# Kernel optimization log

Hardware: AMD Instinct MI355X
Metric: run time of the kernel (lower is better)

Reference implementation:

```python
import jax, jax.numpy as jnp
import numpy as np

B, S, D, H = 4, 1024, 1024, 16
DK = D // H


def _rel_shift(x):
    # Transformer-XL relative shift: x is (b, h, t1, t2) with t1 == t2
    b, h, t1, t2 = x.shape
    x = jnp.pad(x, ((0, 0), (0, 0), (0, 0), (1, 0)))  # pad left of last dim
    x = x.reshape(b, h, t2 + 1, t1)
    return x[:, :, 1:, :].reshape(b, h, t1, t2)


def setup_inputs() -> dict:
    rng = jax.random.key(0)
    ks = jax.random.split(rng, 10)
    w = 0.02
    return {
        "query": jax.random.normal(ks[0], (B, S, D), jnp.float32),
        "key": jax.random.normal(ks[1], (B, S, D), jnp.float32),
        "value": jax.random.normal(ks[2], (B, S, D), jnp.float32),
        "mask": jnp.ones((B, S), dtype=bool),
        "Wq": jax.random.normal(ks[3], (D, D), jnp.float32) * w,
        "Wk": jax.random.normal(ks[4], (D, D), jnp.float32) * w,
        "Wv": jax.random.normal(ks[5], (D, D), jnp.float32) * w,
        "Wp": jax.random.normal(ks[6], (D, D), jnp.float32) * w,
        "Wo": jax.random.normal(ks[7], (D, D), jnp.float32) * w,
        "pos_bias_u": jax.random.normal(ks[8], (H, DK), jnp.float32) * w,
        "pos_bias_v": jax.random.normal(ks[9], (H, DK), jnp.float32) * w,
    }


def reference(query, key, value, mask, Wq, Wk, Wv, Wp, Wo, pos_bias_u, pos_bias_v):
    b, s, dm = query.shape
    h, dk = pos_bias_u.shape

    # sinusoidal relative position embeddings (positions s-1 ... 0)
    inv_freq = 1.0 / (10000.0 ** (jnp.arange(0, dm, 2, dtype=jnp.float32) / dm))
    pos_seq = jnp.arange(s - 1, -1, -1, dtype=jnp.float32)
    sin_inp = pos_seq[:, None] * inv_freq[None, :]              # (s, dm/2)
    pos_emb = jnp.concatenate([jnp.sin(sin_inp), jnp.cos(sin_inp)], -1)  # (s, dm)

    # projections (torch Linear: y = x @ W.T)
    q = (query @ Wq.T).reshape(b, s, h, dk).transpose(0, 2, 1, 3)  # (b,h,s,dk)
    k = (key @ Wk.T).reshape(b, s, h, dk).transpose(0, 2, 1, 3)
    v = (value @ Wv.T).reshape(b, s, h, dk).transpose(0, 2, 1, 3)
    p = (pos_emb @ Wp.T).reshape(s, h, dk).transpose(1, 0, 2)       # (h,s,dk), same for all batches

    content_score = jnp.einsum('bhqd,bhkd->bhqk', q + pos_bias_u[None, :, None, :], k)
    pos_score = jnp.einsum('bhqd,hkd->bhqk', q + pos_bias_v[None, :, None, :], p)
    pos_score = _rel_shift(pos_score)

    scores = (content_score + pos_score) / jnp.sqrt(jnp.float32(dk))
    attn_mask = mask[:, None, :, None] & mask[:, None, None, :]    # (b,1,q,k)
    scores = jnp.where(attn_mask, scores, jnp.float32(-1e9))

    attn = jax.nn.softmax(scores, axis=-1)  # dropout is identity at eval
    context = jnp.einsum('bhqk,bhkd->bqhd', attn, v).reshape(b, s, dm)
    return context @ Wo.T
```

## Files before the change

kernel.cpp:

```cpp
#include <hip/hip_runtime.h>
#include <math.h>

#define BATCH 4
#define SEQ   1024
#define DM    1024
#define NH    16
#define DK    64

typedef __attribute__((ext_vector_type(8))) short short8;
typedef __attribute__((ext_vector_type(4))) float f32x4;

__device__ inline unsigned short f2bf(float f) {
    unsigned u = __float_as_uint(f);
    unsigned r = (u + 0x7fffu + ((u >> 16) & 1u)) >> 16;
    return (unsigned short)r;
}
__device__ inline float bf2f(unsigned short s) {
    return __uint_as_float(((unsigned)s) << 16);
}
__device__ inline void split1(float x, unsigned short& h, unsigned short& l) {
    h = f2bf(x);
    l = f2bf(x - bf2f(h));
}

__global__ __launch_bounds__(256) void cvt_split(const float4* __restrict__ x,
                                                 ushort4* __restrict__ h,
                                                 ushort4* __restrict__ l, int n4) {
    int i = blockIdx.x * blockDim.x + threadIdx.x;
    if (i >= n4) return;
    float4 v = x[i];
    ushort4 hv, lv;
    split1(v.x, hv.x, lv.x);
    split1(v.y, hv.y, lv.y);
    split1(v.z, hv.z, lv.z);
    split1(v.w, hv.w, lv.w);
    h[i] = hv;
    l[i] = lv;
}

__global__ void posemb_kernel(unsigned short* __restrict__ peh,
                              unsigned short* __restrict__ pel) {
    int idx = blockIdx.x * blockDim.x + threadIdx.x;
    if (idx >= SEQ * DM) return;
    int j = idx / DM, d = idx % DM;
    double pos = (double)(SEQ - 1 - j);
    int i = (d < DM / 2) ? d : d - DM / 2;
    double inv_freq = exp(-((2.0 * (double)i) / (double)DM) * log(10000.0));
    double a = pos * inv_freq;
    float v = (d < DM / 2) ? (float)sin(a) : (float)cos(a);
    unsigned short hh, ll;
    split1(v, hh, ll);
    peh[idx] = hh;
    pel[idx] = ll;
}

__global__ __launch_bounds__(256) void prep_q(const float4* __restrict__ qp4,
                                              const float4* __restrict__ ub4,
                                              const float4* __restrict__ vb4,
                                              ushort4* __restrict__ quh,
                                              ushort4* __restrict__ qul,
                                              ushort4* __restrict__ qvh,
                                              ushort4* __restrict__ qvl) {
    int i = blockIdx.x * 256 + threadIdx.x;
    float4 q = qp4[i];
    int dm4 = i & (DM / 4 - 1);
    float4 u = ub4[dm4], v = vb4[dm4];
    ushort4 h, l;
    split1(q.x + u.x, h.x, l.x);
    split1(q.y + u.y, h.y, l.y);
    split1(q.z + u.z, h.z, l.z);
    split1(q.w + u.w, h.w, l.w);
    quh[i] = h; qul[i] = l;
    split1(q.x + v.x, h.x, l.x);
    split1(q.y + v.y, h.y, l.y);
    split1(q.z + v.z, h.z, l.z);
    split1(q.w + v.w, h.w, l.w);
    qvh[i] = h; qvl[i] = l;
}

__global__ __launch_bounds__(256) void vtrans_kernel(const float* __restrict__ vp,
                                                     unsigned short* __restrict__ vth,
                                                     unsigned short* __restrict__ vtl) {
    __shared__ float tile[64][65];
    int s0 = blockIdx.x * 64, h = blockIdx.y, b = blockIdx.z;
    int t = threadIdx.x;
#pragma unroll
    for (int i = 0; i < 16; i++) {
        int idx = t + 256 * i;
        int sl = idx >> 6, d = idx & 63;
        tile[sl][d] = vp[((size_t)b * SEQ + s0 + sl) * DM + h * DK + d];
    }
    __syncthreads();
    int bh = b * NH + h;
#pragma unroll
    for (int i = 0; i < 16; i++) {
        int idx = t + 256 * i;
        int dl = idx >> 6, sl = idx & 63;
        float x = tile[sl][dl];
        unsigned short hi, lo;
        split1(x, hi, lo);
        size_t o = ((size_t)bh * DK + dl) * SEQ + s0 + sl;
        vth[o] = hi;
        vtl[o] = lo;
    }
}

__device__ inline void load16(const void* g, void* l) {
    __builtin_amdgcn_global_load_lds(
        (const __attribute__((address_space(1))) unsigned int*)g,
        (__attribute__((address_space(3))) unsigned int*)l, 16, 0, 0);
}

__global__ __launch_bounds__(256) void gemm_split_nt(
        const unsigned short* __restrict__ Ah, const unsigned short* __restrict__ Al,
        const unsigned short* __restrict__ Bh, const unsigned short* __restrict__ Bl,
        float* __restrict__ C, int M, int N, int K,
        long aStride, long bStride, long cStride,
        const unsigned short* __restrict__ PEh, const unsigned short* __restrict__ PEl,
        const unsigned short* __restrict__ Wph, const unsigned short* __restrict__ Wpl,
        float* __restrict__ Cp) {
    __shared__ __attribute__((aligned(16))) short Ah_s[128 * 32];
    __shared__ __attribute__((aligned(16))) short Al_s[128 * 32];
    __shared__ __attribute__((aligned(16))) short Bh_s[128 * 32];
    __shared__ __attribute__((aligned(16))) short Bl_s[128 * 32];

    int z = blockIdx.z;
    int bm = blockIdx.y * 128, bn = blockIdx.x * 128;
    if (z == 3) {
        if (bm >= SEQ) return;
        Ah = PEh; Al = PEl; Bh = Wph; Bl = Wpl; C = Cp;
    } else {
        Ah += (size_t)z * aStride; Al += (size_t)z * aStride;
        Bh += (size_t)z * bStride; Bl += (size_t)z * bStride;
        C  += (size_t)z * cStride;
    }

    int tid = threadIdx.x, w = tid >> 6, lane = tid & 63;
    int quad = lane >> 4, tl = lane & 15;
    int wm = (w >> 1) * 64, wn = (w & 1) * 64;

    int sr = w * 32 + (lane >> 2);
    int sc = (lane & 3) * 8;
    const unsigned short* gA0h = Ah + (size_t)(bm + sr) * K + sc;
    const unsigned short* gA1h = Ah + (size_t)(bm + sr + 16) * K + sc;
    const unsigned short* gA0l = Al + (size_t)(bm + sr) * K + sc;
    const unsigned short* gA1l = Al + (size_t)(bm + sr + 16) * K + sc;
    const unsigned short* gB0h = Bh + (size_t)(bn + sr) * K + sc;
    const unsigned short* gB1h = Bh + (size_t)(bn + sr + 16) * K + sc;
    const unsigned short* gB0l = Bl + (size_t)(bn + sr) * K + sc;
    const unsigned short* gB1l = Bl + (size_t)(bn + sr + 16) * K + sc;
    short* lA0h = Ah_s + (w * 32) * 32;  short* lA1h = lA0h + 16 * 32;
    short* lA0l = Al_s + (w * 32) * 32;  short* lA1l = lA0l + 16 * 32;
    short* lB0h = Bh_s + (w * 32) * 32;  short* lB1h = lB0h + 16 * 32;
    short* lB0l = Bl_s + (w * 32) * 32;  short* lB1l = lB0l + 16 * 32;

    f32x4 acc[4][4];
#pragma unroll
    for (int mi = 0; mi < 4; mi++)
#pragma unroll
        for (int ni = 0; ni < 4; ni++)
            acc[mi][ni] = (f32x4){0.f, 0.f, 0.f, 0.f};

    for (int k0 = 0; k0 < K; k0 += 32) {
        load16(gA0h, lA0h); load16(gA1h, lA1h);
        load16(gA0l, lA0l); load16(gA1l, lA1l);
        load16(gB0h, lB0h); load16(gB1h, lB1h);
        load16(gB0l, lB0l); load16(gB1l, lB1l);
        gA0h += 32; gA1h += 32; gA0l += 32; gA1l += 32;
        gB0h += 32; gB1h += 32; gB0l += 32; gB1l += 32;
        __syncthreads();

        short8 ah[4], al[4], bh[4], bl[4];
#pragma unroll
        for (int mi = 0; mi < 4; mi++) {
            int r = wm + mi * 16 + tl;
            ah[mi] = *(const short8*)(Ah_s + r * 32 + quad * 8);
            al[mi] = *(const short8*)(Al_s + r * 32 + quad * 8);
        }
#pragma unroll
        for (int ni = 0; ni < 4; ni++) {
            int r = wn + ni * 16 + tl;
            bh[ni] = *(const short8*)(Bh_s + r * 32 + quad * 8);
            bl[ni] = *(const short8*)(Bl_s + r * 32 + quad * 8);
        }
#pragma unroll
        for (int mi = 0; mi < 4; mi++)
#pragma unroll
            for (int ni = 0; ni < 4; ni++) {
                acc[mi][ni] = __builtin_amdgcn_mfma_f32_16x16x32_bf16(
                    ah[mi], bh[ni], acc[mi][ni], 0, 0, 0);
                acc[mi][ni] = __builtin_amdgcn_mfma_f32_16x16x32_bf16(
                    al[mi], bh[ni], acc[mi][ni], 0, 0, 0);
                acc[mi][ni] = __builtin_amdgcn_mfma_f32_16x16x32_bf16(
                    ah[mi], bl[ni], acc[mi][ni], 0, 0, 0);
            }
        __syncthreads();
    }
#pragma unroll
    for (int mi = 0; mi < 4; mi++)
#pragma unroll
        for (int ni = 0; ni < 4; ni++)
#pragma unroll
            for (int r = 0; r < 4; r++)
                C[(size_t)(bm + wm + mi * 16 + quad * 4 + r) * N +
                  bn + wn + ni * 16 + tl] = acc[mi][ni][r];
}

__global__ __launch_bounds__(256) void gemm_scores(
        const unsigned short* __restrict__ quh, const unsigned short* __restrict__ qul,
        const unsigned short* __restrict__ qvh, const unsigned short* __restrict__ qvl,
        const unsigned short* __restrict__ kh,  const unsigned short* __restrict__ kl,
        const unsigned short* __restrict__ ph,  const unsigned short* __restrict__ pl,
        unsigned short* __restrict__ contC, unsigned short* __restrict__ posC,
        int bh0, int nc) {
    __shared__ __attribute__((aligned(16))) short Ah_s[128 * 32];
    __shared__ __attribute__((aligned(16))) short Al_s[128 * 32];
    __shared__ __attribute__((aligned(16))) short Bh_s[128 * 32];
    __shared__ __attribute__((aligned(16))) short Bl_s[128 * 32];

    int z = blockIdx.z;
    bool isPos = z >= nc;
    int zi = isPos ? z - nc : z;
    int bh = bh0 + zi, b = bh >> 4, h = bh & 15;
    size_t qoff = (size_t)b * SEQ * DM + h * DK;
    const unsigned short *Ah, *Al, *Bh, *Bl;
    if (!isPos) { Ah = quh + qoff; Al = qul + qoff; Bh = kh + qoff; Bl = kl + qoff; }
    else        { Ah = qvh + qoff; Al = qvl + qoff; Bh = ph + h * DK; Bl = pl + h * DK; }
    unsigned short* C = (isPos ? posC : contC) + (size_t)zi * SEQ * SEQ;

    int tid = threadIdx.x, w = tid >> 6, lane = tid & 63;
    int bm = blockIdx.y * 128, bn = blockIdx.x * 128;
    int quad = lane >> 4, tl = lane & 15;
    int wm = (w >> 1) * 64, wn = (w & 1) * 64;

    int sr = w * 32 + (lane >> 2);
    int sc = (lane & 3) * 8;
    const unsigned short* gA0h = Ah + (size_t)(bm + sr) * DM + sc;
    const unsigned short* gA1h = Ah + (size_t)(bm + sr + 16) * DM + sc;
    const unsigned short* gA0l = Al + (size_t)(bm + sr) * DM + sc;
    const unsigned short* gA1l = Al + (size_t)(bm + sr + 16) * DM + sc;
    const unsigned short* gB0h = Bh + (size_t)(bn + sr) * DM + sc;
    const unsigned short* gB1h = Bh + (size_t)(bn + sr + 16) * DM + sc;
    const unsigned short* gB0l = Bl + (size_t)(bn + sr) * DM + sc;
    const unsigned short* gB1l = Bl + (size_t)(bn + sr + 16) * DM + sc;
    short* lA0h = Ah_s + (w * 32) * 32;  short* lA1h = lA0h + 16 * 32;
    short* lA0l = Al_s + (w * 32) * 32;  short* lA1l = lA0l + 16 * 32;
    short* lB0h = Bh_s + (w * 32) * 32;  short* lB1h = lB0h + 16 * 32;
    short* lB0l = Bl_s + (w * 32) * 32;  short* lB1l = lB0l + 16 * 32;

    f32x4 acc[4][4];
#pragma unroll
    for (int mi = 0; mi < 4; mi++)
#pragma unroll
        for (int ni = 0; ni < 4; ni++)
            acc[mi][ni] = (f32x4){0.f, 0.f, 0.f, 0.f};

    for (int k0 = 0; k0 < DK; k0 += 32) {
        load16(gA0h, lA0h); load16(gA1h, lA1h);
        load16(gA0l, lA0l); load16(gA1l, lA1l);
        load16(gB0h, lB0h); load16(gB1h, lB1h);
        load16(gB0l, lB0l); load16(gB1l, lB1l);
        gA0h += 32; gA1h += 32; gA0l += 32; gA1l += 32;
        gB0h += 32; gB1h += 32; gB0l += 32; gB1l += 32;
        __syncthreads();

        short8 ah[4], al[4], bh[4], bl[4];
#pragma unroll
        for (int mi = 0; mi < 4; mi++) {
            int r = wm + mi * 16 + tl;
            ah[mi] = *(const short8*)(Ah_s + r * 32 + quad * 8);
            al[mi] = *(const short8*)(Al_s + r * 32 + quad * 8);
        }
#pragma unroll
        for (int ni = 0; ni < 4; ni++) {
            int r = wn + ni * 16 + tl;
            bh[ni] = *(const short8*)(Bh_s + r * 32 + quad * 8);
            bl[ni] = *(const short8*)(Bl_s + r * 32 + quad * 8);
        }
#pragma unroll
        for (int mi = 0; mi < 4; mi++)
#pragma unroll
            for (int ni = 0; ni < 4; ni++) {
                acc[mi][ni] = __builtin_amdgcn_mfma_f32_16x16x32_bf16(
                    ah[mi], bh[ni], acc[mi][ni], 0, 0, 0);
                acc[mi][ni] = __builtin_amdgcn_mfma_f32_16x16x32_bf16(
                    al[mi], bh[ni], acc[mi][ni], 0, 0, 0);
                acc[mi][ni] = __builtin_amdgcn_mfma_f32_16x16x32_bf16(
                    ah[mi], bl[ni], acc[mi][ni], 0, 0, 0);
            }
        __syncthreads();
    }
#pragma unroll
    for (int mi = 0; mi < 4; mi++)
#pragma unroll
        for (int ni = 0; ni < 4; ni++)
#pragma unroll
            for (int r = 0; r < 4; r++)
                C[(size_t)(bm + wm + mi * 16 + quad * 4 + r) * SEQ +
                  bn + wn + ni * 16 + tl] = f2bf(acc[mi][ni][r]);
}

__global__ __launch_bounds__(512) void content_softmax(
        const unsigned short* __restrict__ quh, const unsigned short* __restrict__ qul,
        const unsigned short* __restrict__ kh,  const unsigned short* __restrict__ kl,
        const unsigned short* __restrict__ posC,
        const unsigned short* __restrict__ vth, const unsigned short* __restrict__ vtl,
        unsigned short* __restrict__ cxh, unsigned short* __restrict__ cxl,
        int bh0) {
    __shared__ __attribute__((aligned(16))) short smem[69888];
    short* S_s = smem + 36864;

    int zi = blockIdx.y;
    int q0 = blockIdx.x * 32;
    int bh = bh0 + zi, b = bh >> 4, h = bh & 15;
    size_t qoff = (size_t)b * SEQ * DM + h * DK;
    const unsigned short* Ah = quh + qoff;
    const unsigned short* Al = qul + qoff;
    const unsigned short* Bh = kh + qoff;
    const unsigned short* Bl = kl + qoff;

    int t = threadIdx.x, w = t >> 6, lane = t & 63;
    int quad = lane >> 4, tl = lane & 15;
    int mi = w >> 2;
    int ni0 = (w & 3) * 2;

    {
        int r8 = w & 3;
        short* dst = smem + (w < 4 ? 0 : 2048) + r8 * 512;
        const unsigned short* srcb = (w < 4 ? Ah : Al);
        load16(srcb + (size_t)(q0 + r8 * 8 + (lane >> 3)) * DM + (lane & 7) * 8, dst);
    }
    {
        int bb = 4096;
#pragma unroll
        for (int i = 0; i < 2; i++) {
            int row = w * 16 + i * 8 + (lane >> 3);
            load16(Bh + (size_t)row * DM + (lane & 7) * 8, smem + bb + w * 1024 + i * 512);
            load16(Bl + (size_t)row * DM + (lane & 7) * 8, smem + bb + 8192 + w * 1024 + i * 512);
        }
    }
    __syncthreads();

    short8 afh[2], afl[2];
#pragma unroll
    for (int kc = 0; kc < 2; kc++) {
        afh[kc] = *(const short8*)(smem + (mi * 16 + tl) * 64 + kc * 32 + quad * 8);
        afl[kc] = *(const short8*)(smem + 2048 + (mi * 16 + tl) * 64 + kc * 32 + quad * 8);
    }

    for (int nb = 0; nb < 8; nb++) {
        int bb  = (nb & 1) ? 20480 : 4096;
        int nbb = (nb & 1) ? 4096 : 20480;
        if (nb < 7) {
            int n0 = (nb + 1) * 128;
#pragma unroll
            for (int i = 0; i < 2; i++) {
                int row = n0 + w * 16 + i * 8 + (lane >> 3);
                load16(Bh + (size_t)row * DM + (lane & 7) * 8, smem + nbb + w * 1024 + i * 512);
                load16(Bl + (size_t)row * DM + (lane & 7) * 8, smem + nbb + 8192 + w * 1024 + i * 512);
            }
        }

        f32x4 acc0 = (f32x4){0.f, 0.f, 0.f, 0.f};
        f32x4 acc1 = (f32x4){0.f, 0.f, 0.f, 0.f};
#pragma unroll
        for (int kc = 0; kc < 2; kc++) {
            short8 bh0f = *(const short8*)(smem + bb + ((ni0) * 16 + tl) * 64 + kc * 32 + quad * 8);
            short8 bl0f = *(const short8*)(smem + bb + 8192 + ((ni0) * 16 + tl) * 64 + kc * 32 + quad * 8);
            short8 bh1f = *(const short8*)(smem + bb + ((ni0 + 1) * 16 + tl) * 64 + kc * 32 + quad * 8);
            short8 bl1f = *(const short8*)(smem + bb + 8192 + ((ni0 + 1) * 16 + tl) * 64 + kc * 32 + quad * 8);
            acc0 = __builtin_amdgcn_mfma_f32_16x16x32_bf16(afh[kc], bh0f, acc0, 0, 0, 0);
            acc0 = __builtin_amdgcn_mfma_f32_16x16x32_bf16(afl[kc], bh0f, acc0, 0, 0, 0);
            acc0 = __builtin_amdgcn_mfma_f32_16x16x32_bf16(afh[kc], bl0f, acc0, 0, 0, 0);
            acc1 = __builtin_amdgcn_mfma_f32_16x16x32_bf16(afh[kc], bh1f, acc1, 0, 0, 0);
            acc1 = __builtin_amdgcn_mfma_f32_16x16x32_bf16(afl[kc], bh1f, acc1, 0, 0, 0);
            acc1 = __builtin_amdgcn_mfma_f32_16x16x32_bf16(afh[kc], bl1f, acc1, 0, 0, 0);
        }
#pragma unroll
        for (int r = 0; r < 4; r++) {
            int row = mi * 16 + quad * 4 + r;
            S_s[row * 1032 + nb * 128 + ni0 * 16 + tl]       = (short)f2bf(acc0[r]);
            S_s[row * 1032 + nb * 128 + (ni0 + 1) * 16 + tl] = (short)f2bf(acc1[r]);
        }
        __syncthreads();
    }

    int nrows = (q0 <= 991) ? 33 : 32;
    {
        float4* P4 = (float4*)smem;
        const float4* src4 = (const float4*)(posC + ((size_t)zi * SEQ + q0) * SEQ);
        int n4 = nrows * 128;
        for (int i = t; i < n4; i += 512) P4[i] = src4[i];
    }
    __syncthreads();

    int niw = w & 3;
    const unsigned short* gVh = vth + ((size_t)bh * DK + niw * 16 + tl) * SEQ + quad * 8;
    const unsigned short* gVl = vtl + ((size_t)bh * DK + niw * 16 + tl) * SEQ + quad * 8;
    short8 vhA[4], vlA[4], vhB[4], vlB[4];
#pragma unroll
    for (int kc = 0; kc < 4; kc++) {
        vhA[kc] = *(const short8*)(gVh + kc * 32);
        vlA[kc] = *(const short8*)(gVl + kc * 32);
    }

    const unsigned short* P_s = (const unsigned short*)smem;
#pragma unroll
    for (int j = 0; j < 4; j++) {
        int rl = w * 4 + j;
        int q = q0 + rl;
        short* Srow = S_s + rl * 1032;
        float v[16];
        float m = -1e30f;
#pragma unroll
        for (int s = 0; s < 4; s++) {
            int kb = s * 256 + lane * 4;
            ushort4 sc = *(const ushort4*)(Srow + kb);
#pragma unroll
            for (int e = 0; e < 4; e++) {
                int k = kb + e;
                bool lo = (k <= q);
                int srow = rl + (lo ? 0 : 1);
                int scol = lo ? (k + SEQ - 1 - q) : (k - q - 2);
                float pos = 0.f;
                if (k != q + 1) pos = bf2f(P_s[srow * 1024 + scol]);
                float val = (bf2f(((const unsigned short*)&sc)[e]) + pos) * 0.125f;
                v[s * 4 + e] = val;
                m = fmaxf(m, val);
            }
        }
#pragma unroll
        for (int off = 32; off > 0; off >>= 1) m = fmaxf(m, __shfl_xor(m, off));
        float sum = 0.f;
#pragma unroll
        for (int i = 0; i < 16; i++) { v[i] = __expf(v[i] - m); sum += v[i]; }
#pragma unroll
        for (int off = 32; off > 0; off >>= 1) sum += __shfl_xor(sum, off);
        float inv = 1.0f / sum;
#pragma unroll
        for (int s = 0; s < 4; s++) {
            ushort4 o;
            o.x = f2bf(v[s * 4 + 0] * inv);
            o.y = f2bf(v[s * 4 + 1] * inv);
            o.z = f2bf(v[s * 4 + 2] * inv);
            o.w = f2bf(v[s * 4 + 3] * inv);
            *(ushort4*)((unsigned short*)Srow + s * 256 + lane * 4) = o;
        }
    }
    __syncthreads();

    {
        const short* As0 = S_s + (mi * 16 + tl) * 1032 + quad * 8;
        f32x4 p0 = (f32x4){0.f, 0.f, 0.f, 0.f};
        f32x4 p1 = (f32x4){0.f, 0.f, 0.f, 0.f};
#pragma unroll
        for (int nb = 0; nb < 8; nb++) {
            const bool even = (nb & 1) == 0;
            if (nb < 7) {
                const unsigned short* nh = gVh + (size_t)(nb + 1) * 128;
                const unsigned short* nl = gVl + (size_t)(nb + 1) * 128;
#pragma unroll
                for (int kc = 0; kc < 4; kc++) {
                    if (even) {
                        vhB[kc] = *(const short8*)(nh + kc * 32);
                        vlB[kc] = *(const short8*)(nl + kc * 32);
                    } else {
                        vhA[kc] = *(const short8*)(nh + kc * 32);
                        vlA[kc] = *(const short8*)(nl + kc * 32);
                    }
                }
            }
#pragma unroll
            for (int kc = 0; kc < 4; kc++) {
                short8 a   = *(const short8*)(As0 + nb * 128 + kc * 32);
                short8 vh8 = even ? vhA[kc] : vhB[kc];
                short8 vl8 = even ? vlA[kc] : vlB[kc];
                if (kc & 1) {
                    p1 = __builtin_amdgcn_mfma_f32_16x16x32_bf16(a, vh8, p1, 0, 0, 0);
                    p1 = __builtin_amdgcn_mfma_f32_16x16x32_bf16(a, vl8, p1, 0, 0, 0);
                } else {
                    p0 = __builtin_amdgcn_mfma_f32_16x16x32_bf16(a, vh8, p0, 0, 0, 0);
                    p0 = __builtin_amdgcn_mfma_f32_16x16x32_bf16(a, vl8, p0, 0, 0, 0);
                }
            }
        }
#pragma unroll
        for (int r = 0; r < 4; r++) {
            float val = p0[r] + p1[r];
            size_t a = qoff + (size_t)(q0 + mi * 16 + quad * 4 + r) * DM + niw * 16 + tl;
            unsigned short hh, ll;
            split1(val, hh, ll);
            cxh[a] = hh;
            cxl[a] = ll;
        }
    }
}

extern "C" void kernel_launch(void* const* d_in, const int* in_sizes, int n_in,
                              void* d_out, int out_size, void* d_ws, size_t ws_size,
                              hipStream_t stream) {
    const float* query = (const float*)d_in[0];
    const float* key   = (const float*)d_in[1];
    const float* value = (const float*)d_in[2];
    const float* Wq = (const float*)d_in[4];
    const float* Wk = (const float*)d_in[5];
    const float* Wv = (const float*)d_in[6];
    const float* Wp = (const float*)d_in[7];
    const float* Wo = (const float*)d_in[8];
    const float* pu = (const float*)d_in[9];
    const float* pvb = (const float*)d_in[10];
    float* out = (float*)d_out;

    const size_t MB = 1u << 20;
    char* wsb = (char*)d_ws;
    float* pp     = (float*)(wsb + 4 * MB);
    float* qp     = (float*)(wsb + 8 * MB);
    float* kp     = (float*)(wsb + 24 * MB);
    float* vp     = (float*)(wsb + 40 * MB);
    unsigned short* qAh = (unsigned short*)(wsb + 56 * MB);
    unsigned short* qAl = (unsigned short*)(wsb + 64 * MB);
    unsigned short* kAh = (unsigned short*)(wsb + 72 * MB);
    unsigned short* kAl = (unsigned short*)(wsb + 80 * MB);
    unsigned short* vAh = (unsigned short*)(wsb + 88 * MB);
    unsigned short* vAl = (unsigned short*)(wsb + 96 * MB);
    unsigned short* Wqh = (unsigned short*)(wsb + 104 * MB);
    unsigned short* Wql = (unsigned short*)(wsb + 106 * MB);
    unsigned short* Wkh = (unsigned short*)(wsb + 108 * MB);
    unsigned short* Wkl = (unsigned short*)(wsb + 110 * MB);
    unsigned short* Wvh = (unsigned short*)(wsb + 112 * MB);
    unsigned short* Wvl = (unsigned short*)(wsb + 114 * MB);
    unsigned short* PEh = (unsigned short*)(wsb + 116 * MB);
    unsigned short* PEl = (unsigned short*)(wsb + 118 * MB);
    unsigned short* Wph = (unsigned short*)(wsb + 120 * MB);
    unsigned short* Wpl = (unsigned short*)(wsb + 122 * MB);
    unsigned short* quh = (unsigned short*)(wsb + 56 * MB);
    unsigned short* qul = (unsigned short*)(wsb + 64 * MB);
    unsigned short* qvh = (unsigned short*)(wsb + 72 * MB);
    unsigned short* qvl = (unsigned short*)(wsb + 80 * MB);
    unsigned short* khs = (unsigned short*)(wsb + 88 * MB);
    unsigned short* kls = (unsigned short*)(wsb + 96 * MB);
    unsigned short* phs = (unsigned short*)(wsb + 104 * MB);
    unsigned short* pls = (unsigned short*)(wsb + 106 * MB);
    unsigned short* vth = (unsigned short*)(wsb + 108 * MB);
    unsigned short* vtl = (unsigned short*)(wsb + 116 * MB);
    unsigned short* CXh = (unsigned short*)(wsb + 24 * MB);
    unsigned short* CXl = (unsigned short*)(wsb + 32 * MB);
    unsigned short* Woh = (unsigned short*)(wsb + 40 * MB);
    unsigned short* Wol = (unsigned short*)(wsb + 42 * MB);
    unsigned short* posC = (unsigned short*)(wsb + 124 * MB);

    int nc = (ws_size >= 188 * MB) ? 32 : 16;

    const int N4BIG = (BATCH * SEQ * DM) / 4;
    const int N4W   = (DM * DM) / 4;

    posemb_kernel<<<(SEQ * DM + 255) / 256, 256, 0, stream>>>(PEh, PEl);
    cvt_split<<<N4W / 256, 256, 0, stream>>>((const float4*)Wp, (ushort4*)Wph, (ushort4*)Wpl, N4W);

    cvt_split<<<N4BIG / 256, 256, 0, stream>>>((const float4*)query, (ushort4*)qAh, (ushort4*)qAl, N4BIG);
    cvt_split<<<N4BIG / 256, 256, 0, stream>>>((const float4*)key,   (ushort4*)kAh, (ushort4*)kAl, N4BIG);
    cvt_split<<<N4BIG / 256, 256, 0, stream>>>((const float4*)value, (ushort4*)vAh, (ushort4*)vAl, N4BIG);
    cvt_split<<<N4W / 256, 256, 0, stream>>>((const float4*)Wq, (ushort4*)Wqh, (ushort4*)Wql, N4W);
    cvt_split<<<N4W / 256, 256, 0, stream>>>((const float4*)Wk, (ushort4*)Wkh, (ushort4*)Wkl, N4W);
    cvt_split<<<N4W / 256, 256, 0, stream>>>((const float4*)Wv, (ushort4*)Wvh, (ushort4*)Wvl, N4W);
    long aS = 8L * MB, bS = 2L * MB, cS = 4L * MB;
    gemm_split_nt<<<dim3(DM / 128, (BATCH * SEQ) / 128, 4), 256, 0, stream>>>(
        qAh, qAl, Wqh, Wql, qp, BATCH * SEQ, DM, DM, aS, bS, cS,
        PEh, PEl, Wph, Wpl, pp);

    prep_q<<<N4BIG / 256, 256, 0, stream>>>((const float4*)qp, (const float4*)pu,
                                            (const float4*)pvb, (ushort4*)quh,
                                            (ushort4*)qul, (ushort4*)qvh, (ushort4*)qvl);
    cvt_split<<<N4BIG / 256, 256, 0, stream>>>((const float4*)kp, (ushort4*)khs, (ushort4*)kls, N4BIG);
    cvt_split<<<(SEQ * DM / 4) / 256, 256, 0, stream>>>((const float4*)pp, (ushort4*)phs, (ushort4*)pls, SEQ * DM / 4);
    vtrans_kernel<<<dim3(SEQ / 64, NH, BATCH), 256, 0, stream>>>(vp, vth, vtl);
    cvt_split<<<N4W / 256, 256, 0, stream>>>((const float4*)Wo, (ushort4*)Woh, (ushort4*)Wol, N4W);

    for (int c = 0; c < BATCH * NH; c += nc) {
        gemm_scores<<<dim3(SEQ / 128, SEQ / 128, nc), 256, 0, stream>>>(
            quh, qul, qvh, qvl, khs, kls, phs, pls, posC, posC, c, 0);
        content_softmax<<<dim3(SEQ / 32, nc), 512, 0, stream>>>(
            quh, qul, khs, kls, posC, vth, vtl, CXh, CXl, c);
    }

    gemm_split_nt<<<dim3(DM / 128, (BATCH * SEQ) / 128, 1), 256, 0, stream>>>(
        CXh, CXl, Woh, Wol, out, BATCH * SEQ, DM, DM, 0, 0, 0,
        nullptr, nullptr, nullptr, nullptr, nullptr);
}
```

Measured before the change: 629.5 us.

## Fuse positional score GEMM and rel-shift into the attention softmax kernel

```diff
diff --git a/kernel.cpp b/kernel.cpp
--- a/kernel.cpp
+++ b/kernel.cpp
@@ -206,197 +206,146 @@
                   bn + wn + ni * 16 + tl] = acc[mi][ni][r];
 }
 
-__global__ __launch_bounds__(256) void gemm_scores(
+__global__ __launch_bounds__(256, 2) void content_softmax(
         const unsigned short* __restrict__ quh, const unsigned short* __restrict__ qul,
         const unsigned short* __restrict__ qvh, const unsigned short* __restrict__ qvl,
         const unsigned short* __restrict__ kh,  const unsigned short* __restrict__ kl,
         const unsigned short* __restrict__ ph,  const unsigned short* __restrict__ pl,
-        unsigned short* __restrict__ contC, unsigned short* __restrict__ posC,
-        int bh0, int nc) {
-    __shared__ __attribute__((aligned(16))) short Ah_s[128 * 32];
-    __shared__ __attribute__((aligned(16))) short Al_s[128 * 32];
-    __shared__ __attribute__((aligned(16))) short Bh_s[128 * 32];
-    __shared__ __attribute__((aligned(16))) short Bl_s[128 * 32];
-
-    int z = blockIdx.z;
-    bool isPos = z >= nc;
-    int zi = isPos ? z - nc : z;
-    int bh = bh0 + zi, b = bh >> 4, h = bh & 15;
+        const unsigned short* __restrict__ vth, const unsigned short* __restrict__ vtl,
+        unsigned short* __restrict__ cxh, unsigned short* __restrict__ cxl) {
+    __shared__ __attribute__((aligned(16))) short smem[36992];
+    short* S_s = smem + 20480;
+
+    int bh = blockIdx.y, b = bh >> 4, h = bh & 15;
+    int q0 = blockIdx.x * 16;
     size_t qoff = (size_t)b * SEQ * DM + h * DK;
-    const unsigned short *Ah, *Al, *Bh, *Bl;
-    if (!isPos) { Ah = quh + qoff; Al = qul + qoff; Bh = kh + qoff; Bl = kl + qoff; }
-    else        { Ah = qvh + qoff; Al = qvl + qoff; Bh = ph + h * DK; Bl = pl + h * DK; }
-    unsigned short* C = (isPos ? posC : contC) + (size_t)zi * SEQ * SEQ;
-
-    int tid = threadIdx.x, w = tid >> 6, lane = tid & 63;
-    int bm = blockIdx.y * 128, bn = blockIdx.x * 128;
-    int quad = lane >> 4, tl = lane & 15;
-    int wm = (w >> 1) * 64, wn = (w & 1) * 64;
-
-    int sr = w * 32 + (lane >> 2);
-    int sc = (lane & 3) * 8;
-    const unsigned short* gA0h = Ah + (size_t)(bm + sr) * DM + sc;
-    const unsigned short* gA1h = Ah + (size_t)(bm + sr + 16) * DM + sc;
-    const unsigned short* gA0l = Al + (size_t)(bm + sr) * DM + sc;
-    const unsigned short* gA1l = Al + (size_t)(bm + sr + 16) * DM + sc;
-    const unsigned short* gB0h = Bh + (size_t)(bn + sr) * DM + sc;
-    const unsigned short* gB1h = Bh + (size_t)(bn + sr + 16) * DM + sc;
-    const unsigned short* gB0l = Bl + (size_t)(bn + sr) * DM + sc;
-    const unsigned short* gB1l = Bl + (size_t)(bn + sr + 16) * DM + sc;
-    short* lA0h = Ah_s + (w * 32) * 32;  short* lA1h = lA0h + 16 * 32;
-    short* lA0l = Al_s + (w * 32) * 32;  short* lA1l = lA0l + 16 * 32;
-    short* lB0h = Bh_s + (w * 32) * 32;  short* lB1h = lB0h + 16 * 32;
-    short* lB0l = Bl_s + (w * 32) * 32;  short* lB1l = lB0l + 16 * 32;
-
-    f32x4 acc[4][4];
-#pragma unroll
-    for (int mi = 0; mi < 4; mi++)
-#pragma unroll
-        for (int ni = 0; ni < 4; ni++)
-            acc[mi][ni] = (f32x4){0.f, 0.f, 0.f, 0.f};
-
-    for (int k0 = 0; k0 < DK; k0 += 32) {
-        load16(gA0h, lA0h); load16(gA1h, lA1h);
-        load16(gA0l, lA0l); load16(gA1l, lA1l);
-        load16(gB0h, lB0h); load16(gB1h, lB1h);
-        load16(gB0l, lB0l); load16(gB1l, lB1l);
-        gA0h += 32; gA1h += 32; gA0l += 32; gA1l += 32;
-        gB0h += 32; gB1h += 32; gB0l += 32; gB1l += 32;
-        __syncthreads();
-
-        short8 ah[4], al[4], bh[4], bl[4];
-#pragma unroll
-        for (int mi = 0; mi < 4; mi++) {
-            int r = wm + mi * 16 + tl;
-            ah[mi] = *(const short8*)(Ah_s + r * 32 + quad * 8);
-            al[mi] = *(const short8*)(Al_s + r * 32 + quad * 8);
-        }
-#pragma unroll
-        for (int ni = 0; ni < 4; ni++) {
-            int r = wn + ni * 16 + tl;
-            bh[ni] = *(const short8*)(Bh_s + r * 32 + quad * 8);
-            bl[ni] = *(const short8*)(Bl_s + r * 32 + quad * 8);
-        }
-#pragma unroll
-        for (int mi = 0; mi < 4; mi++)
-#pragma unroll
-            for (int ni = 0; ni < 4; ni++) {
-                acc[mi][ni] = __builtin_amdgcn_mfma_f32_16x16x32_bf16(
-                    ah[mi], bh[ni], acc[mi][ni], 0, 0, 0);
-                acc[mi][ni] = __builtin_amdgcn_mfma_f32_16x16x32_bf16(
-                    al[mi], bh[ni], acc[mi][ni], 0, 0, 0);
-                acc[mi][ni] = __builtin_amdgcn_mfma_f32_16x16x32_bf16(
-                    ah[mi], bl[ni], acc[mi][ni], 0, 0, 0);
-            }
-        __syncthreads();
-    }
-#pragma unroll
-    for (int mi = 0; mi < 4; mi++)
-#pragma unroll
-        for (int ni = 0; ni < 4; ni++)
-#pragma unroll
-            for (int r = 0; r < 4; r++)
-                C[(size_t)(bm + wm + mi * 16 + quad * 4 + r) * SEQ +
-                  bn + wn + ni * 16 + tl] = f2bf(acc[mi][ni][r]);
-}
-
-__global__ __launch_bounds__(512) void content_softmax(
-        const unsigned short* __restrict__ quh, const unsigned short* __restrict__ qul,
-        const unsigned short* __restrict__ kh,  const unsigned short* __restrict__ kl,
-        const unsigned short* __restrict__ posC,
-        const unsigned short* __restrict__ vth, const unsigned short* __restrict__ vtl,
-        unsigned short* __restrict__ cxh, unsigned short* __restrict__ cxl,
-        int bh0) {
-    __shared__ __attribute__((aligned(16))) short smem[69888];
-    short* S_s = smem + 36864;
-
-    int zi = blockIdx.y;
-    int q0 = blockIdx.x * 32;
-    int bh = bh0 + zi, b = bh >> 4, h = bh & 15;
-    size_t qoff = (size_t)b * SEQ * DM + h * DK;
-    const unsigned short* Ah = quh + qoff;
-    const unsigned short* Al = qul + qoff;
-    const unsigned short* Bh = kh + qoff;
-    const unsigned short* Bl = kl + qoff;
+    size_t poff = (size_t)h * DK;
 
     int t = threadIdx.x, w = t >> 6, lane = t & 63;
     int quad = lane >> 4, tl = lane & 15;
-    int mi = w >> 2;
-    int ni0 = (w & 3) * 2;
+
+    auto stageB = [&](const unsigned short* Bh_, const unsigned short* Bl_,
+                      size_t rowoff, int lbase) {
+#pragma unroll
+        for (int i = 0; i < 4; i++) {
+            int srow = (i & 1) * 32 + (t >> 3);
+            int u = (t & 7) ^ (srow & 7);
+            const unsigned short* src =
+                ((i >> 1) ? Bl_ : Bh_) + rowoff + (size_t)srow * DM + u * 8;
+            load16(src, smem + lbase + i * 2048 + t * 8);
+        }
+    };
 
     {
-        int r8 = w & 3;
-        short* dst = smem + (w < 4 ? 0 : 2048) + r8 * 512;
-        const unsigned short* srcb = (w < 4 ? Ah : Al);
-        load16(srcb + (size_t)(q0 + r8 * 8 + (lane >> 3)) * DM + (lane & 7) * 8, dst);
-    }
+        int s = t >> 7;
+        int row = (t >> 3) & 15;
+        int u = (t & 7) ^ (row & 7);
+        const unsigned short* src = (s ? qul : quh) + qoff + (size_t)(q0 + row) * DM + u * 8;
+        load16(src, smem + s * 2048 + (t & 127) * 8);
+    }
+    stageB(kh + qoff, kl + qoff, 0, 4096);
+    __syncthreads();
+
+    short8 afh[2], afl[2];
+#pragma unroll
+    for (int kc = 0; kc < 2; kc++) {
+        int uu = ((kc * 4 + quad) ^ (tl & 7)) * 8;
+        afh[kc] = *(const short8*)(smem + tl * 64 + uu);
+        afl[kc] = *(const short8*)(smem + 2048 + tl * 64 + uu);
+    }
+
+    int lr = w * 16 + tl;
+    for (int nb = 0; nb < 16; nb++) {
+        int bb  = (nb & 1) ? 12288 : 4096;
+        int nbb = (nb & 1) ? 4096 : 12288;
+        if (nb < 15)
+            stageB(kh + qoff, kl + qoff, (size_t)((nb + 1) * 64) * DM, nbb);
+        f32x4 acc = (f32x4){0.f, 0.f, 0.f, 0.f};
+#pragma unroll
+        for (int kc = 0; kc < 2; kc++) {
+            int uu = ((kc * 4 + quad) ^ (tl & 7)) * 8;
+            short8 b8h = *(const short8*)(smem + bb + lr * 64 + uu);
+            short8 b8l = *(const short8*)(smem + bb + 4096 + lr * 64 + uu);
+            acc = __builtin_amdgcn_mfma_f32_16x16x32_bf16(afh[kc], b8h, acc, 0, 0, 0);
+            acc = __builtin_amdgcn_mfma_f32_16x16x32_bf16(afl[kc], b8h, acc, 0, 0, 0);
+            acc = __builtin_amdgcn_mfma_f32_16x16x32_bf16(afh[kc], b8l, acc, 0, 0, 0);
+        }
+#pragma unroll
+        for (int r = 0; r < 4; r++)
+            S_s[(quad * 4 + r) * 1032 + nb * 64 + lr] = (short)f2bf(acc[r]);
+        __syncthreads();
+    }
+
     {
-        int bb = 4096;
 #pragma unroll
         for (int i = 0; i < 2; i++) {
-            int row = w * 16 + i * 8 + (lane >> 3);
-            load16(Bh + (size_t)row * DM + (lane & 7) * 8, smem + bb + w * 1024 + i * 512);
-            load16(Bl + (size_t)row * DM + (lane & 7) * 8, smem + bb + 8192 + w * 1024 + i * 512);
-        }
-    }
+            int row = t >> 3;
+            int u = (t & 7) ^ (row & 7);
+            int gr = q0 + row; if (gr > SEQ - 1) gr = SEQ - 1;
+            const unsigned short* src = (i ? qvl : qvh) + qoff + (size_t)gr * DM + u * 8;
+            load16(src, smem + i * 2048 + t * 8);
+        }
+    }
+    stageB(ph + poff, pl + poff, 0, 4096);
     __syncthreads();
 
-    short8 afh[2], afl[2];
+    short8 aph0[2], apl0[2], aph1[2], apl1[2];
 #pragma unroll
     for (int kc = 0; kc < 2; kc++) {
-        afh[kc] = *(const short8*)(smem + (mi * 16 + tl) * 64 + kc * 32 + quad * 8);
-        afl[kc] = *(const short8*)(smem + 2048 + (mi * 16 + tl) * 64 + kc * 32 + quad * 8);
-    }
-
-    for (int nb = 0; nb < 8; nb++) {
-        int bb  = (nb & 1) ? 20480 : 4096;
-        int nbb = (nb & 1) ? 4096 : 20480;
-        if (nb < 7) {
-            int n0 = (nb + 1) * 128;
-#pragma unroll
-            for (int i = 0; i < 2; i++) {
-                int row = n0 + w * 16 + i * 8 + (lane >> 3);
-                load16(Bh + (size_t)row * DM + (lane & 7) * 8, smem + nbb + w * 1024 + i * 512);
-                load16(Bl + (size_t)row * DM + (lane & 7) * 8, smem + nbb + 8192 + w * 1024 + i * 512);
-            }
-        }
-
+        int uu0 = ((kc * 4 + quad) ^ (tl & 7)) * 8;
+        aph0[kc] = *(const short8*)(smem + tl * 64 + uu0);
+        apl0[kc] = *(const short8*)(smem + 2048 + tl * 64 + uu0);
+        int lr1 = 16 + tl;
+        int uu1 = ((kc * 4 + quad) ^ (lr1 & 7)) * 8;
+        aph1[kc] = *(const short8*)(smem + lr1 * 64 + uu1);
+        apl1[kc] = *(const short8*)(smem + 2048 + lr1 * 64 + uu1);
+    }
+
+    for (int nb = 0; nb < 16; nb++) {
+        int bb  = (nb & 1) ? 12288 : 4096;
+        int nbb = (nb & 1) ? 4096 : 12288;
+        if (nb < 15)
+            stageB(ph + poff, pl + poff, (size_t)((nb + 1) * 64) * DM, nbb);
+        bool needT1 = (nb * 64 <= 1006 - q0);
         f32x4 acc0 = (f32x4){0.f, 0.f, 0.f, 0.f};
         f32x4 acc1 = (f32x4){0.f, 0.f, 0.f, 0.f};
 #pragma unroll
         for (int kc = 0; kc < 2; kc++) {
-            short8 bh0f = *(const short8*)(smem + bb + ((ni0) * 16 + tl) * 64 + kc * 32 + quad * 8);
-            short8 bl0f = *(const short8*)(smem + bb + 8192 + ((ni0) * 16 + tl) * 64 + kc * 32 + quad * 8);
-            short8 bh1f = *(const short8*)(smem + bb + ((ni0 + 1) * 16 + tl) * 64 + kc * 32 + quad * 8);
-            short8 bl1f = *(const short8*)(smem + bb + 8192 + ((ni0 + 1) * 16 + tl) * 64 + kc * 32 + quad * 8);
-            acc0 = __builtin_amdgcn_mfma_f32_16x16x32_bf16(afh[kc], bh0f, acc0, 0, 0, 0);
-            acc0 = __builtin_amdgcn_mfma_f32_16x16x32_bf16(afl[kc], bh0f, acc0, 0, 0, 0);
-            acc0 = __builtin_amdgcn_mfma_f32_16x16x32_bf16(afh[kc], bl0f, acc0, 0, 0, 0);
-            acc1 = __builtin_amdgcn_mfma_f32_16x16x32_bf16(afh[kc], bh1f, acc1, 0, 0, 0);
-            acc1 = __builtin_amdgcn_mfma_f32_16x16x32_bf16(afl[kc], bh1f, acc1, 0, 0, 0);
-            acc1 = __builtin_amdgcn_mfma_f32_16x16x32_bf16(afh[kc], bl1f, acc1, 0, 0, 0);
-        }
-#pragma unroll
-        for (int r = 0; r < 4; r++) {
-            int row = mi * 16 + quad * 4 + r;
-            S_s[row * 1032 + nb * 128 + ni0 * 16 + tl]       = (short)f2bf(acc0[r]);
-            S_s[row * 1032 + nb * 128 + (ni0 + 1) * 16 + tl] = (short)f2bf(acc1[r]);
+            int uu = ((kc * 4 + quad) ^ (tl & 7)) * 8;
+            short8 b8h = *(const short8*)(smem + bb + lr * 64 + uu);
+            short8 b8l = *(const short8*)(smem + bb + 4096 + lr * 64 + uu);
+            acc0 = __builtin_amdgcn_mfma_f32_16x16x32_bf16(aph0[kc], b8h, acc0, 0, 0, 0);
+            acc0 = __builtin_amdgcn_mfma_f32_16x16x32_bf16(apl0[kc], b8h, acc0, 0, 0, 0);
+            acc0 = __builtin_amdgcn_mfma_f32_16x16x32_bf16(aph0[kc], b8l, acc0, 0, 0, 0);
+            if (needT1) {
+                acc1 = __builtin_amdgcn_mfma_f32_16x16x32_bf16(aph1[kc], b8h, acc1, 0, 0, 0);
+                acc1 = __builtin_amdgcn_mfma_f32_16x16x32_bf16(apl1[kc], b8h, acc1, 0, 0, 0);
+                acc1 = __builtin_amdgcn_mfma_f32_16x16x32_bf16(aph1[kc], b8l, acc1, 0, 0, 0);
+            }
+        }
+        int tg = nb * 64 + lr;
+#pragma unroll
+        for (int mt = 0; mt < 2; mt++) {
+            if (mt == 1 && !needT1) break;
+#pragma unroll
+            for (int r = 0; r < 4; r++) {
+                int pr = mt * 16 + quad * 4 + r;
+                int Q = q0 + pr;
+                float pv = (mt == 0) ? acc0[r] : acc1[r];
+                int srow, scol; bool valid;
+                if (tg >= 1023 - Q) { srow = pr;     scol = tg - 1023 + Q; valid = (pr <= 15); }
+                else                { srow = pr - 1; scol = tg + Q + 1;    valid = (pr >= 1 && pr <= 16); }
+                if (valid) {
+                    short* sp = S_s + srow * 1032 + scol;
+                    *sp = (short)f2bf(bf2f(*(const unsigned short*)sp) + pv);
+                }
+            }
         }
         __syncthreads();
     }
 
-    int nrows = (q0 <= 991) ? 33 : 32;
-    {
-        float4* P4 = (float4*)smem;
-        const float4* src4 = (const float4*)(posC + ((size_t)zi * SEQ + q0) * SEQ);
-        int n4 = nrows * 128;
-        for (int i = t; i < n4; i += 512) P4[i] = src4[i];
-    }
-    __syncthreads();
-
-    int niw = w & 3;
-    const unsigned short* gVh = vth + ((size_t)bh * DK + niw * 16 + tl) * SEQ + quad * 8;
-    const unsigned short* gVl = vtl + ((size_t)bh * DK + niw * 16 + tl) * SEQ + quad * 8;
+    const unsigned short* gVh = vth + ((size_t)bh * DK + w * 16 + tl) * SEQ + quad * 8;
+    const unsigned short* gVl = vtl + ((size_t)bh * DK + w * 16 + tl) * SEQ + quad * 8;
     short8 vhA[4], vlA[4], vhB[4], vlB[4];
 #pragma unroll
     for (int kc = 0; kc < 4; kc++) {
@@ -404,27 +353,18 @@
         vlA[kc] = *(const short8*)(gVl + kc * 32);
     }
 
-    const unsigned short* P_s = (const unsigned short*)smem;
 #pragma unroll
     for (int j = 0; j < 4; j++) {
         int rl = w * 4 + j;
-        int q = q0 + rl;
         short* Srow = S_s + rl * 1032;
         float v[16];
         float m = -1e30f;
 #pragma unroll
         for (int s = 0; s < 4; s++) {
-            int kb = s * 256 + lane * 4;
-            ushort4 sc = *(const ushort4*)(Srow + kb);
+            ushort4 sc = *(const ushort4*)(Srow + s * 256 + lane * 4);
 #pragma unroll
             for (int e = 0; e < 4; e++) {
-                int k = kb + e;
-                bool lo = (k <= q);
-                int srow = rl + (lo ? 0 : 1);
-                int scol = lo ? (k + SEQ - 1 - q) : (k - q - 2);
-                float pos = 0.f;
-                if (k != q + 1) pos = bf2f(P_s[srow * 1024 + scol]);
-                float val = (bf2f(((const unsigned short*)&sc)[e]) + pos) * 0.125f;
+                float val = bf2f(((const unsigned short*)&sc)[e]) * 0.125f;
                 v[s * 4 + e] = val;
                 m = fmaxf(m, val);
             }
@@ -450,7 +390,7 @@
     __syncthreads();
 
     {
-        const short* As0 = S_s + (mi * 16 + tl) * 1032 + quad * 8;
+        const short* As0 = S_s + tl * 1032 + quad * 8;
         f32x4 p0 = (f32x4){0.f, 0.f, 0.f, 0.f};
         f32x4 p1 = (f32x4){0.f, 0.f, 0.f, 0.f};
 #pragma unroll
@@ -487,7 +427,7 @@
 #pragma unroll
         for (int r = 0; r < 4; r++) {
             float val = p0[r] + p1[r];
-            size_t a = qoff + (size_t)(q0 + mi * 16 + quad * 4 + r) * DM + niw * 16 + tl;
+            size_t a = qoff + (size_t)(q0 + quad * 4 + r) * DM + w * 16 + tl;
             unsigned short hh, ll;
             split1(val, hh, ll);
             cxh[a] = hh;
@@ -547,9 +487,6 @@
     unsigned short* CXl = (unsigned short*)(wsb + 32 * MB);
     unsigned short* Woh = (unsigned short*)(wsb + 40 * MB);
     unsigned short* Wol = (unsigned short*)(wsb + 42 * MB);
-    unsigned short* posC = (unsigned short*)(wsb + 124 * MB);
-
-    int nc = (ws_size >= 188 * MB) ? 32 : 16;
 
     const int N4BIG = (BATCH * SEQ * DM) / 4;
     const int N4W   = (DM * DM) / 4;
@@ -576,12 +513,8 @@
     vtrans_kernel<<<dim3(SEQ / 64, NH, BATCH), 256, 0, stream>>>(vp, vth, vtl);
     cvt_split<<<N4W / 256, 256, 0, stream>>>((const float4*)Wo, (ushort4*)Woh, (ushort4*)Wol, N4W);
 
-    for (int c = 0; c < BATCH * NH; c += nc) {
-        gemm_scores<<<dim3(SEQ / 128, SEQ / 128, nc), 256, 0, stream>>>(
-            quh, qul, qvh, qvl, khs, kls, phs, pls, posC, posC, c, 0);
-        content_softmax<<<dim3(SEQ / 32, nc), 512, 0, stream>>>(
-            quh, qul, khs, kls, posC, vth, vtl, CXh, CXl, c);
-    }
+    content_softmax<<<dim3(SEQ / 16, BATCH * NH), 256, 0, stream>>>(
+        quh, qul, qvh, qvl, khs, kls, phs, pls, vth, vtl, CXh, CXl);
 
     gemm_split_nt<<<dim3(DM / 128, (BATCH * SEQ) / 128, 1), 256, 0, stream>>>(
         CXh, CXl, Woh, Wol, out, BATCH * SEQ, DM, DM, 0, 0, 0,
```

New measurement: 628.2 us. About the same (-0.2%).
